# Kernel tuning notes

Measured on AMD Instinct MI355X. Metric: run time of the kernel, lower is better.

Reference implementation:

```python
import jax, jax.numpy as jnp
import numpy as np


def setup_inputs() -> dict:
    key = jax.random.key(0)
    ks = jax.random.split(key, 9)
    N, K, CS, CT, OUT, S = 50000, 16, 64, 64, 64, 4
    x = jax.random.normal(ks[0], (N, CT), dtype=jnp.float32)
    src = jax.random.normal(ks[1], (N, CS), dtype=jnp.float32)
    neighbor_idx = jax.random.randint(ks[2], (N, K), 0, N, dtype=jnp.int32)
    scale_t = 1.0 / np.sqrt(CT)
    scale_s = 1.0 / np.sqrt(CS)
    Wt = jax.random.normal(ks[3], (CT, S), dtype=jnp.float32) * scale_t
    bt = jax.random.normal(ks[4], (S,), dtype=jnp.float32) * scale_t
    Ws = jax.random.normal(ks[5], (CS, S), dtype=jnp.float32) * scale_s
    bs = jax.random.normal(ks[6], (S,), dtype=jnp.float32) * scale_s
    W_lin = jax.random.normal(ks[7], (S, CS, OUT), dtype=jnp.float32) * scale_s
    b_lin = jax.random.normal(ks[8], (S, OUT), dtype=jnp.float32) * scale_s
    return {"x": x, "src": src, "neighbor_idx": neighbor_idx,
            "Wt": Wt, "bt": bt, "Ws": Ws, "bs": bs,
            "W_lin": W_lin, "b_lin": b_lin}


def reference(x, src, neighbor_idx, Wt, bt, Ws, bs, W_lin, b_lin):
    # Gather per-node neighbor messages: [N, K, Cs]
    msgs = src[neighbor_idx]
    size = Wt.shape[-1]
    # target assignment logits from own data: [N, S]
    t = x @ Wt + bt
    # source assignment logits from messages: [N, K, S]
    s = jnp.einsum('nkc,cs->nks', msgs, Ws) + bs
    # soft assignment over the `size` weight matrices (softmax over S)
    a = jax.nn.softmax(s + t[:, None, :], axis=-1)  # [N, K, S]
    # apply each of the `size` linears to the messages: [N, K, S, O]
    w = jnp.einsum('nkc,sco->nkso', msgs, W_lin) + b_lin
    # assignment-weighted mean over the S weight matrices: [N, K, O]
    out = jnp.einsum('nks,nkso->nko', a, w) / size
    return out
```

## Files before the change

kernel.cpp:

```cpp
#include <hip/hip_runtime.h>

#define CT 64
#define CS 64
#define K_NB 16
#define S_SZ 4
#define OUT_C 64

__global__ __launch_bounds__(256) void k0_logits(
    const float* __restrict__ x, const float* __restrict__ src,
    const float* __restrict__ Wt, const float* __restrict__ bt,
    const float* __restrict__ Ws, const float* __restrict__ bs,
    float* __restrict__ t_out, float* __restrict__ sl_out, int N)
{
    int r = blockIdx.x * blockDim.x + threadIdx.x;
    if (r >= N) return;
    const float4* xv  = (const float4*)(x   + (size_t)r * CT);
    const float4* sv  = (const float4*)(src + (size_t)r * CS);
    const float4* Wt4 = (const float4*)Wt;
    const float4* Ws4 = (const float4*)Ws;
    float4 at = *(const float4*)bt;
    float4 as = *(const float4*)bs;
    #pragma unroll
    for (int c4 = 0; c4 < 16; ++c4) {
        float4 xq = xv[c4];
        float4 sq = sv[c4];
        float xs_[4] = {xq.x, xq.y, xq.z, xq.w};
        float ss_[4] = {sq.x, sq.y, sq.z, sq.w};
        #pragma unroll
        for (int u = 0; u < 4; ++u) {
            float4 wt = Wt4[c4 * 4 + u];
            float4 ws = Ws4[c4 * 4 + u];
            at.x = fmaf(xs_[u], wt.x, at.x);
            at.y = fmaf(xs_[u], wt.y, at.y);
            at.z = fmaf(xs_[u], wt.z, at.z);
            at.w = fmaf(xs_[u], wt.w, at.w);
            as.x = fmaf(ss_[u], ws.x, as.x);
            as.y = fmaf(ss_[u], ws.y, as.y);
            as.z = fmaf(ss_[u], ws.z, as.z);
            as.w = fmaf(ss_[u], ws.w, as.w);
        }
    }
    ((float4*)t_out)[r]  = at;
    ((float4*)sl_out)[r] = as;
}

__global__ __launch_bounds__(256, 4) void k1_z(
    const float* __restrict__ src, const float* __restrict__ W_lin,
    const float* __restrict__ b_lin, float* __restrict__ Z, int N)
{
    const int col = threadIdx.x;
    const int s = col >> 6, o = col & 63;
    float w[64];
    #pragma unroll
    for (int c = 0; c < 64; ++c)
        w[c] = W_lin[s * 4096 + (c << 6) + o];
    const float bl = b_lin[col];
    __shared__ float lsrc[64];
    for (int j = blockIdx.x; j < N; j += gridDim.x) {
        if (threadIdx.x < 16)
            ((float4*)lsrc)[threadIdx.x] =
                ((const float4*)(src + ((size_t)j << 6)))[threadIdx.x];
        __syncthreads();
        const float4* l4 = (const float4*)lsrc;
        float a0 = bl, a1 = 0.f, a2 = 0.f, a3 = 0.f;
        #pragma unroll
        for (int c4 = 0; c4 < 16; ++c4) {
            float4 s4 = l4[c4];
            a0 = fmaf(s4.x, w[c4 * 4 + 0], a0);
            a1 = fmaf(s4.y, w[c4 * 4 + 1], a1);
            a2 = fmaf(s4.z, w[c4 * 4 + 2], a2);
            a3 = fmaf(s4.w, w[c4 * 4 + 3], a3);
        }
        Z[(size_t)j * 256 + col] = (a0 + a1) + (a2 + a3);
        __syncthreads();
    }
}

__global__ __launch_bounds__(256) void k2_out(
    const int* __restrict__ nidx, const float* __restrict__ t_in,
    const float* __restrict__ sl_in, const float* __restrict__ Z,
    float* __restrict__ out)
{
    const int T = blockIdx.x * 256 + threadIdx.x;
    const int p = T >> 4;
    const int quad = T & 15;
    const int n = p >> 4;
    const int j = nidx[p];
    float4 tv = ((const float4*)t_in)[n];
    float4 sv = ((const float4*)sl_in)[j];
    float l0 = tv.x + sv.x, l1 = tv.y + sv.y;
    float l2 = tv.z + sv.z, l3 = tv.w + sv.w;
    float m = fmaxf(fmaxf(l0, l1), fmaxf(l2, l3));
    float e0 = __expf(l0 - m), e1 = __expf(l1 - m);
    float e2 = __expf(l2 - m), e3 = __expf(l3 - m);
    float inv = 0.25f / (e0 + e1 + e2 + e3);
    const float4* zb = (const float4*)Z + (size_t)j * 64 + quad;
    float4 z0 = zb[0], z1 = zb[16], z2 = zb[32], z3 = zb[48];
    float4 o;
    o.x = (e0 * z0.x + e1 * z1.x + e2 * z2.x + e3 * z3.x) * inv;
    o.y = (e0 * z0.y + e1 * z1.y + e2 * z2.y + e3 * z3.y) * inv;
    o.z = (e0 * z0.z + e1 * z1.z + e2 * z2.z + e3 * z3.z) * inv;
    o.w = (e0 * z0.w + e1 * z1.w + e2 * z2.w + e3 * z3.w) * inv;
    ((float4*)out)[(size_t)p * 16 + quad] = o;
}

extern "C" void kernel_launch(void* const* d_in, const int* in_sizes, int n_in,
                              void* d_out, int out_size, void* d_ws, size_t ws_size,
                              hipStream_t stream)
{
    const float* x   = (const float*)d_in[0];
    const float* src = (const float*)d_in[1];
    const int*   idx = (const int*)d_in[2];
    const float* Wt  = (const float*)d_in[3];
    const float* bt  = (const float*)d_in[4];
    const float* Ws  = (const float*)d_in[5];
    const float* bs  = (const float*)d_in[6];
    const float* Wl  = (const float*)d_in[7];
    const float* bl  = (const float*)d_in[8];
    float* out = (float*)d_out;

    const int N = in_sizes[0] / CT;

    float* Z  = (float*)d_ws;
    float* t  = Z + (size_t)N * 256;
    float* sl = t + (size_t)N * 4;

    hipLaunchKernelGGL(k0_logits, dim3((N + 255) / 256), dim3(256), 0, stream,
                       x, src, Wt, bt, Ws, bs, t, sl, N);
    hipLaunchKernelGGL(k1_z, dim3(1024), dim3(256), 0, stream,
                       src, Wl, bl, Z, N);
    hipLaunchKernelGGL(k2_out, dim3(N), dim3(256), 0, stream,
                       idx, t, sl, Z, out);
}
```

Baseline: 413.0 us.

## Store Z table in fp16, fuse logits into Z kernel, nontemporal output stores

Stores the per-node projected table Z as half precision, which halves the bytes written in the Z pass and gathered in the output pass. Merges the logit kernel into the Z kernel, so eight threads per row also compute the target and source logits, and drops the shared-memory staging and barriers in favour of direct row loads. The output is written with nontemporal stores. The price is reduced precision in Z, which may exceed the tolerance, and a serial 64-step logit loop on a few threads inside the main loop.

```diff
diff --git a/kernel.cpp b/kernel.cpp
--- a/kernel.cpp
+++ b/kernel.cpp
@@ -1,4 +1,5 @@
 #include <hip/hip_runtime.h>
+#include <hip/hip_fp16.h>
 
 #define CT 64
 #define CS 64
@@ -6,47 +7,15 @@
 #define S_SZ 4
 #define OUT_C 64
 
-__global__ __launch_bounds__(256) void k0_logits(
+typedef float vf4 __attribute__((ext_vector_type(4)));
+
+__global__ __launch_bounds__(256, 4) void k1_all(
     const float* __restrict__ x, const float* __restrict__ src,
     const float* __restrict__ Wt, const float* __restrict__ bt,
     const float* __restrict__ Ws, const float* __restrict__ bs,
-    float* __restrict__ t_out, float* __restrict__ sl_out, int N)
-{
-    int r = blockIdx.x * blockDim.x + threadIdx.x;
-    if (r >= N) return;
-    const float4* xv  = (const float4*)(x   + (size_t)r * CT);
-    const float4* sv  = (const float4*)(src + (size_t)r * CS);
-    const float4* Wt4 = (const float4*)Wt;
-    const float4* Ws4 = (const float4*)Ws;
-    float4 at = *(const float4*)bt;
-    float4 as = *(const float4*)bs;
-    #pragma unroll
-    for (int c4 = 0; c4 < 16; ++c4) {
-        float4 xq = xv[c4];
-        float4 sq = sv[c4];
-        float xs_[4] = {xq.x, xq.y, xq.z, xq.w};
-        float ss_[4] = {sq.x, sq.y, sq.z, sq.w};
-        #pragma unroll
-        for (int u = 0; u < 4; ++u) {
-            float4 wt = Wt4[c4 * 4 + u];
-            float4 ws = Ws4[c4 * 4 + u];
-            at.x = fmaf(xs_[u], wt.x, at.x);
-            at.y = fmaf(xs_[u], wt.y, at.y);
-            at.z = fmaf(xs_[u], wt.z, at.z);
-            at.w = fmaf(xs_[u], wt.w, at.w);
-            as.x = fmaf(ss_[u], ws.x, as.x);
-            as.y = fmaf(ss_[u], ws.y, as.y);
-            as.z = fmaf(ss_[u], ws.z, as.z);
-            as.w = fmaf(ss_[u], ws.w, as.w);
-        }
-    }
-    ((float4*)t_out)[r]  = at;
-    ((float4*)sl_out)[r] = as;
-}
-
-__global__ __launch_bounds__(256, 4) void k1_z(
-    const float* __restrict__ src, const float* __restrict__ W_lin,
-    const float* __restrict__ b_lin, float* __restrict__ Z, int N)
+    const float* __restrict__ W_lin, const float* __restrict__ b_lin,
+    __half* __restrict__ Zh, float* __restrict__ t_out,
+    float* __restrict__ sl_out, int N)
 {
     const int col = threadIdx.x;
     const int s = col >> 6, o = col & 63;
@@ -55,30 +24,38 @@
     for (int c = 0; c < 64; ++c)
         w[c] = W_lin[s * 4096 + (c << 6) + o];
     const float bl = b_lin[col];
-    __shared__ float lsrc[64];
+
     for (int j = blockIdx.x; j < N; j += gridDim.x) {
-        if (threadIdx.x < 16)
-            ((float4*)lsrc)[threadIdx.x] =
-                ((const float4*)(src + ((size_t)j << 6)))[threadIdx.x];
-        __syncthreads();
-        const float4* l4 = (const float4*)lsrc;
+        const float4* row4 = (const float4*)(src + ((size_t)j << 6));
         float a0 = bl, a1 = 0.f, a2 = 0.f, a3 = 0.f;
         #pragma unroll
         for (int c4 = 0; c4 < 16; ++c4) {
-            float4 s4 = l4[c4];
-            a0 = fmaf(s4.x, w[c4 * 4 + 0], a0);
-            a1 = fmaf(s4.y, w[c4 * 4 + 1], a1);
-            a2 = fmaf(s4.z, w[c4 * 4 + 2], a2);
-            a3 = fmaf(s4.w, w[c4 * 4 + 3], a3);
+            float4 r = row4[c4];
+            a0 = fmaf(r.x, w[c4 * 4 + 0], a0);
+            a1 = fmaf(r.y, w[c4 * 4 + 1], a1);
+            a2 = fmaf(r.z, w[c4 * 4 + 2], a2);
+            a3 = fmaf(r.w, w[c4 * 4 + 3], a3);
         }
-        Z[(size_t)j * 256 + col] = (a0 + a1) + (a2 + a3);
-        __syncthreads();
+        Zh[(size_t)j * 256 + col] = __float2half((a0 + a1) + (a2 + a3));
+
+        if (threadIdx.x < 8) {
+            const int q = threadIdx.x, ss = q & 3;
+            const float* rp = (q < 4) ? (x + ((size_t)j << 6))
+                                      : (src + ((size_t)j << 6));
+            const float* Wp = (q < 4) ? Wt : Ws;
+            float acc = (q < 4) ? bt[ss] : bs[ss];
+            #pragma unroll
+            for (int c = 0; c < 64; ++c)
+                acc = fmaf(rp[c], Wp[c * 4 + ss], acc);
+            if (q < 4) t_out[(size_t)j * 4 + ss] = acc;
+            else       sl_out[(size_t)j * 4 + ss] = acc;
+        }
     }
 }
 
 __global__ __launch_bounds__(256) void k2_out(
     const int* __restrict__ nidx, const float* __restrict__ t_in,
-    const float* __restrict__ sl_in, const float* __restrict__ Z,
+    const float* __restrict__ sl_in, const __half* __restrict__ Zh,
     float* __restrict__ out)
 {
     const int T = blockIdx.x * 256 + threadIdx.x;
@@ -94,14 +71,23 @@
     float e0 = __expf(l0 - m), e1 = __expf(l1 - m);
     float e2 = __expf(l2 - m), e3 = __expf(l3 - m);
     float inv = 0.25f / (e0 + e1 + e2 + e3);
-    const float4* zb = (const float4*)Z + (size_t)j * 64 + quad;
-    float4 z0 = zb[0], z1 = zb[16], z2 = zb[32], z3 = zb[48];
-    float4 o;
-    o.x = (e0 * z0.x + e1 * z1.x + e2 * z2.x + e3 * z3.x) * inv;
-    o.y = (e0 * z0.y + e1 * z1.y + e2 * z2.y + e3 * z3.y) * inv;
-    o.z = (e0 * z0.z + e1 * z1.z + e2 * z2.z + e3 * z3.z) * inv;
-    o.w = (e0 * z0.w + e1 * z1.w + e2 * z2.w + e3 * z3.w) * inv;
-    ((float4*)out)[(size_t)p * 16 + quad] = o;
+
+    const __half2* zb = (const __half2*)Zh + (size_t)j * 128 + quad * 2;
+    __half2 z0a = zb[0],  z0b = zb[1];
+    __half2 z1a = zb[32], z1b = zb[33];
+    __half2 z2a = zb[64], z2b = zb[65];
+    __half2 z3a = zb[96], z3b = zb[97];
+    float2 f0a = __half22float2(z0a), f0b = __half22float2(z0b);
+    float2 f1a = __half22float2(z1a), f1b = __half22float2(z1b);
+    float2 f2a = __half22float2(z2a), f2b = __half22float2(z2b);
+    float2 f3a = __half22float2(z3a), f3b = __half22float2(z3b);
+
+    vf4 o;
+    o.x = (e0 * f0a.x + e1 * f1a.x + e2 * f2a.x + e3 * f3a.x) * inv;
+    o.y = (e0 * f0a.y + e1 * f1a.y + e2 * f2a.y + e3 * f3a.y) * inv;
+    o.z = (e0 * f0b.x + e1 * f1b.x + e2 * f2b.x + e3 * f3b.x) * inv;
+    o.w = (e0 * f0b.y + e1 * f1b.y + e2 * f2b.y + e3 * f3b.y) * inv;
+    __builtin_nontemporal_store(o, (vf4*)out + (size_t)p * 16 + quad);
 }
 
 extern "C" void kernel_launch(void* const* d_in, const int* in_sizes, int n_in,
@@ -121,14 +107,12 @@
 
     const int N = in_sizes[0] / CT;
 
-    float* Z  = (float*)d_ws;
-    float* t  = Z + (size_t)N * 256;
-    float* sl = t + (size_t)N * 4;
+    __half* Zh = (__half*)d_ws;
+    float*  t  = (float*)(Zh + (size_t)N * 256);
+    float*  sl = t + (size_t)N * 4;
 
-    hipLaunchKernelGGL(k0_logits, dim3((N + 255) / 256), dim3(256), 0, stream,
-                       x, src, Wt, bt, Ws, bs, t, sl, N);
-    hipLaunchKernelGGL(k1_z, dim3(1024), dim3(256), 0, stream,
-                       src, Wl, bl, Z, N);
+    hipLaunchKernelGGL(k1_all, dim3(1024), dim3(256), 0, stream,
+                       x, src, Wt, bt, Ws, bs, Wl, bl, Zh, t, sl, N);
     hipLaunchKernelGGL(k2_out, dim3(N), dim3(256), 0, stream,
-                       idx, t, sl, Z, out);
+                       idx, t, sl, Zh, out);
 }
```

Measured after the change: 599.3 us. 45.1% more time.
